# Performance work log

Hardware: AMD Instinct MI355X
Metric: run time of the kernel (lower is better)

The kernel has to match this reference:

```python
import jax, jax.numpy as jnp
import numpy as np

NUM_HEADS = 4
HEAD_DIM = 64
BN_EPS = 1e-5

def _leaky_relu(x, slope=0.2):
    return jnp.where(x >= 0, x, slope * x)

def _gat_conv(x, W, a_src, a_dst, src, dst):
    # x: [N, F_in], W: [F_out, F_in], a_*: [H, D]; edges src/dst: [E]
    N = x.shape[0]
    h = (x @ W.T).reshape(N, NUM_HEADS, HEAD_DIM)          # [N, H, D]
    s_src = jnp.einsum('nhd,hd->nh', h, a_src)              # [N, H]
    s_dst = jnp.einsum('nhd,hd->nh', h, a_dst)              # [N, H]
    e = _leaky_relu(s_src[src] + s_dst[dst])                # [E, H]
    # segment softmax over edges grouped by dst; torch index_reduce_ starts
    # from zeros (include_self=True) -> max with 0
    e_max = jnp.maximum(jax.ops.segment_max(e, dst, num_segments=N), 0.0)
    e_exp = jnp.exp(e - e_max[dst])                         # [E, H]
    e_sum = jax.ops.segment_sum(e_exp, dst, num_segments=N) # [N, H]
    alpha = e_exp / jnp.maximum(e_sum[dst], 1e-9)           # [E, H]
    msg = h[src] * alpha[..., None]                         # [E, H, D]
    out = jax.ops.segment_sum(msg, dst, num_segments=N)     # [N, H, D]
    return out.reshape(N, NUM_HEADS * HEAD_DIM)

def _bn_eval(x, gamma, beta, mean, var):
    return (x - mean) * jax.lax.rsqrt(var + BN_EPS) * gamma + beta

def _elu(x):
    return jnp.where(x > 0, x, jnp.expm1(x))

def setup_inputs() -> dict:
    key = jax.random.key(0)
    ks = jax.random.split(key, 12)
    N, E, IN, HID, OUT = 50000, 500000, 256, 256, 64
    s = 0.05
    return {
        'x': jax.random.normal(ks[0], (N, IN), jnp.float32),
        'edge_index': jax.random.randint(ks[1], (2, E), 0, N, jnp.int64),
        'W1': jax.random.normal(ks[2], (HID, IN), jnp.float32) * s,
        'a_src1': jax.random.normal(ks[3], (NUM_HEADS, HEAD_DIM), jnp.float32) * s,
        'a_dst1': jax.random.normal(ks[4], (NUM_HEADS, HEAD_DIM), jnp.float32) * s,
        'bn1_gamma': jnp.ones((HID,), jnp.float32),
        'bn1_beta': jnp.zeros((HID,), jnp.float32),
        'bn1_mean': jnp.zeros((HID,), jnp.float32),
        'bn1_var': jnp.ones((HID,), jnp.float32),
        'W2': jax.random.normal(ks[5], (HID, HID), jnp.float32) * s,
        'a_src2': jax.random.normal(ks[6], (NUM_HEADS, HEAD_DIM), jnp.float32) * s,
        'a_dst2': jax.random.normal(ks[7], (NUM_HEADS, HEAD_DIM), jnp.float32) * s,
        'bn2_gamma': jnp.ones((HID,), jnp.float32),
        'bn2_beta': jnp.zeros((HID,), jnp.float32),
        'bn2_mean': jnp.zeros((HID,), jnp.float32),
        'bn2_var': jnp.ones((HID,), jnp.float32),
        'Wc': jax.random.normal(ks[8], (OUT, HID), jnp.float32) * s,
        'bc': jnp.zeros((OUT,), jnp.float32),
    }

def reference(x, edge_index, W1, a_src1, a_dst1, bn1_gamma, bn1_beta, bn1_mean, bn1_var,
              W2, a_src2, a_dst2, bn2_gamma, bn2_beta, bn2_mean, bn2_var, Wc, bc):
    src, dst = edge_index[0], edge_index[1]
    h = _gat_conv(x, W1, a_src1, a_dst1, src, dst)
    h = _elu(_bn_eval(h, bn1_gamma, bn1_beta, bn1_mean, bn1_var))
    h = _gat_conv(h, W2, a_src2, a_dst2, src, dst)
    h = _elu(_bn_eval(h, bn2_gamma, bn2_beta, bn2_mean, bn2_var))
    return h @ Wc.T + bc
```

## Files before the change

kernel.cpp:

```cpp
#include <hip/hip_runtime.h>

typedef __attribute__((ext_vector_type(8))) short short8;
typedef __attribute__((ext_vector_type(4))) float f32x4;

#define FF 256
#define NHEAD 4
#define HDIM 64
#define LDS_PITCH 264

__device__ __forceinline__ float bf2f(unsigned short u) {
  union { unsigned u; float f; } v; v.u = ((unsigned)u) << 16; return v.f;
}
__device__ __forceinline__ unsigned short f2bf(float f) {
  union { unsigned u; float f; } v; v.f = f;
  unsigned r = v.u + 0x7FFFu + ((v.u >> 16) & 1u);
  return (unsigned short)(r >> 16);
}

__device__ __forceinline__ short8 loadA8(const unsigned short* p) {
  return *(const short8*)p;
}
__device__ __forceinline__ short8 loadA8(const float* p) {
  f32x4 a = *(const f32x4*)p;
  f32x4 b = *(const f32x4*)(p + 4);
  short8 r;
  r[0] = (short)f2bf(a.x); r[1] = (short)f2bf(a.y);
  r[2] = (short)f2bf(a.z); r[3] = (short)f2bf(a.w);
  r[4] = (short)f2bf(b.x); r[5] = (short)f2bf(b.y);
  r[6] = (short)f2bf(b.z); r[7] = (short)f2bf(b.w);
  return r;
}

__global__ __launch_bounds__(256) void cvtw_kernel(
    const float* __restrict__ p0, int n0, const float* __restrict__ p1, int n1,
    const float* __restrict__ p2, int n2,
    unsigned short* __restrict__ o0, unsigned short* __restrict__ o1,
    unsigned short* __restrict__ o2, int* __restrict__ deg, int nz4) {
  int i = blockIdx.x * 256 + threadIdx.x;
  const float* in;
  unsigned short* out;
  int idx;
  if (i < n0) { in = p0; out = o0; idx = i; }
  else if (i < n0 + n1) { in = p1; out = o1; idx = i - n0; }
  else if (i < n0 + n1 + n2) { in = p2; out = o2; idx = i - n0 - n1; }
  else {
    int z = i - n0 - n1 - n2;
    if (z < nz4) ((int4*)deg)[z] = int4{0, 0, 0, 0};
    return;
  }
  f32x4 v = ((const f32x4*)in)[idx];
  ushort4 o;
  o.x = f2bf(v.x); o.y = f2bf(v.y); o.z = f2bf(v.z); o.w = f2bf(v.w);
  ((ushort4*)out)[idx] = o;
}

__global__ void hist_kernel(const int* __restrict__ dst, int* __restrict__ deg,
                            int E, int N) {
  int i = blockIdx.x * blockDim.x + threadIdx.x;
  if (i < E) {
    int d = dst[i];
    if ((unsigned)d < (unsigned)N) atomicAdd(&deg[d], 1);
  }
}

__global__ __launch_bounds__(256) void scan_chunks(const int* __restrict__ deg,
                                                   int* __restrict__ excl,
                                                   int* __restrict__ csum, int N) {
  __shared__ int s[256];
  int t = threadIdx.x;
  int base = blockIdx.x * 1024 + t * 4;
  int v[4];
  int sum = 0;
#pragma unroll
  for (int i = 0; i < 4; ++i) {
    v[i] = (base + i < N) ? deg[base + i] : 0;
    sum += v[i];
  }
  s[t] = sum;
  __syncthreads();
  for (int off = 1; off < 256; off <<= 1) {
    int x = (t >= off) ? s[t - off] : 0;
    __syncthreads();
    s[t] += x;
    __syncthreads();
  }
  int run = s[t] - sum;
#pragma unroll
  for (int i = 0; i < 4; ++i) {
    if (base + i < N) excl[base + i] = run;
    run += v[i];
  }
  if (t == 255) csum[blockIdx.x] = s[255];
}

__global__ void finalize_rows(const int* __restrict__ excl, const int* __restrict__ csum,
                              int* __restrict__ row_start, int* __restrict__ cursor,
                              int N, int E) {
  int i = blockIdx.x * blockDim.x + threadIdx.x;
  if (i < N) {
    int chunk = i >> 10;
    int pre = 0;
    for (int k = 0; k < chunk; ++k) pre += csum[k];
    int v = excl[i] + pre;
    row_start[i] = v;
    cursor[i] = v;
  }
  if (i == 0) row_start[N] = E;
}

__global__ void scatter_kernel(const int* __restrict__ src, const int* __restrict__ dst,
                               int* __restrict__ cursor, int* __restrict__ sorted_src,
                               int E, int N) {
  int i = blockIdx.x * blockDim.x + threadIdx.x;
  if (i < E) {
    int d = dst[i];
    int s = src[i];
    if ((unsigned)d < (unsigned)N) {
      int p = atomicAdd(&cursor[d], 1);
      if ((unsigned)p < (unsigned)E)
        sorted_src[p] = ((unsigned)s < (unsigned)N) ? s : 0;
    }
  }
}

template <typename AT>
__global__ __launch_bounds__(256) void gemm_main(const AT* __restrict__ A,
                                                 const unsigned short* __restrict__ B,
                                                 unsigned short* __restrict__ Cb,
                                                 const float* __restrict__ a_src,
                                                 const float* __restrict__ a_dst,
                                                 float* __restrict__ sS,
                                                 float* __restrict__ sD,
                                                 int M) {
  __shared__ unsigned short Atile[64 * LDS_PITCH];
  const int K = 256;
  int tid = threadIdx.x;
  int wave = tid >> 6;
  int lane = tid & 63;
  int row0w = blockIdx.x * 64;
  int col0 = wave * 64;
  int lr = lane & 15;
  int quad = lane >> 4;

  short8 breg[4][8];
  {
    const unsigned short* Bp0 = B + (size_t)(col0 + lr) * K + quad * 8;
#pragma unroll
    for (int t = 0; t < 4; ++t)
#pragma unroll
      for (int kk = 0; kk < 8; ++kk)
        breg[t][kk] = *(const short8*)(Bp0 + (size_t)(16 * t) * K + kk * 32);
  }

  {
#pragma unroll
    for (int pass = 0; pass < 8; ++pass) {
      int c = tid + pass * 256;
      int row = c >> 5;
      int col8 = (c & 31) * 8;
      int grow = row0w + row;
      if (grow >= M) grow = M - 1;
      short8 v = loadA8(A + (size_t)grow * K + col8);
      *(short8*)(&Atile[row * LDS_PITCH + col8]) = v;
    }
  }
  __syncthreads();

  f32x4 acc[4][4];
#pragma unroll
  for (int rt = 0; rt < 4; ++rt)
#pragma unroll
    for (int t = 0; t < 4; ++t) acc[rt][t] = f32x4{0, 0, 0, 0};

#pragma unroll
  for (int kk = 0; kk < 8; ++kk) {
    short8 a[4];
#pragma unroll
    for (int rt = 0; rt < 4; ++rt)
      a[rt] = *(const short8*)(&Atile[(rt * 16 + lr) * LDS_PITCH + quad * 8 + kk * 32]);
#pragma unroll
    for (int rt = 0; rt < 4; ++rt)
#pragma unroll
      for (int t = 0; t < 4; ++t)
        acc[rt][t] = __builtin_amdgcn_mfma_f32_16x16x32_bf16(a[rt], breg[t][kk], acc[rt][t], 0, 0, 0);
  }

#pragma unroll
  for (int rt = 0; rt < 4; ++rt) {
#pragma unroll
    for (int t = 0; t < 4; ++t) {
#pragma unroll
      for (int r = 0; r < 4; ++r) {
        int row = row0w + rt * 16 + quad * 4 + r;
        if (row < M) {
          int col = col0 + 16 * t + lr;
          Cb[(size_t)row * FF + col] = f2bf(acc[rt][t][r]);
        }
      }
    }
  }

  {
    float asv[4], adv[4];
#pragma unroll
    for (int t = 0; t < 4; ++t) {
      asv[t] = a_src[col0 + 16 * t + lr];
      adv[t] = a_dst[col0 + 16 * t + lr];
    }
#pragma unroll
    for (int rt = 0; rt < 4; ++rt) {
#pragma unroll
      for (int r = 0; r < 4; ++r) {
        float ps = acc[rt][0][r] * asv[0] + acc[rt][1][r] * asv[1] +
                   acc[rt][2][r] * asv[2] + acc[rt][3][r] * asv[3];
        float pd = acc[rt][0][r] * adv[0] + acc[rt][1][r] * adv[1] +
                   acc[rt][2][r] * adv[2] + acc[rt][3][r] * adv[3];
#pragma unroll
        for (int sft = 1; sft < 16; sft <<= 1) {
          ps += __shfl_xor(ps, sft);
          pd += __shfl_xor(pd, sft);
        }
        if (lr == 0) {
          int row = row0w + rt * 16 + quad * 4 + r;
          if (row < M) {
            sS[row * NHEAD + wave] = ps;
            sD[row * NHEAD + wave] = pd;
          }
        }
      }
    }
  }
}

__global__ __launch_bounds__(256) void gemm_head(const unsigned short* __restrict__ A,
                                                 const unsigned short* __restrict__ B,
                                                 float* __restrict__ Cf,
                                                 const float* __restrict__ bias,
                                                 int M) {
  const int K = 256;
  int wave = threadIdx.x >> 6;
  int lane = threadIdx.x & 63;
  int row0w = blockIdx.x * 256 + wave * 64;
  if (row0w >= M) return;
  int lr = lane & 15;
  int quad = lane >> 4;

  short8 breg[4][8];
  {
    const unsigned short* Bp0 = B + (size_t)lr * K + quad * 8;
#pragma unroll
    for (int t = 0; t < 4; ++t)
#pragma unroll
      for (int kk = 0; kk < 8; ++kk)
        breg[t][kk] = *(const short8*)(Bp0 + (size_t)(16 * t) * K + kk * 32);
  }

  const unsigned short* Aps[4];
#pragma unroll
  for (int rt = 0; rt < 4; ++rt) {
    int arow = row0w + rt * 16 + lr;
    if (arow >= M) arow = M - 1;
    Aps[rt] = A + (size_t)arow * K + quad * 8;
  }

  f32x4 acc[4][4];
#pragma unroll
  for (int rt = 0; rt < 4; ++rt)
#pragma unroll
    for (int t = 0; t < 4; ++t) acc[rt][t] = f32x4{0, 0, 0, 0};

#pragma unroll
  for (int kk = 0; kk < 8; ++kk) {
    short8 a[4];
#pragma unroll
    for (int rt = 0; rt < 4; ++rt) a[rt] = *(const short8*)(Aps[rt] + kk * 32);
#pragma unroll
    for (int rt = 0; rt < 4; ++rt)
#pragma unroll
      for (int t = 0; t < 4; ++t)
        acc[rt][t] = __builtin_amdgcn_mfma_f32_16x16x32_bf16(a[rt], breg[t][kk], acc[rt][t], 0, 0, 0);
  }

#pragma unroll
  for (int rt = 0; rt < 4; ++rt) {
#pragma unroll
    for (int t = 0; t < 4; ++t) {
#pragma unroll
      for (int r = 0; r < 4; ++r) {
        int row = row0w + rt * 16 + quad * 4 + r;
        if (row < M) {
          int col = 16 * t + lr;
          Cf[(size_t)row * 64 + col] = acc[rt][t][r] + bias[col];
        }
      }
    }
  }
}

__global__ __launch_bounds__(256) void aggregate_kernel(
    const unsigned short* __restrict__ hprev, const float* __restrict__ sS,
    const float* __restrict__ sD, const int* __restrict__ row_start,
    const int* __restrict__ sorted_src, const float* __restrict__ gamma,
    const float* __restrict__ beta, const float* __restrict__ mean,
    const float* __restrict__ var, unsigned short* __restrict__ hout, int N) {
  int wave = threadIdx.x >> 6;
  int lane = threadIdx.x & 63;
  int n = blockIdx.x * 4 + wave;
  if (n >= N) return;
  int hh = lane >> 4;
  int slot = lane & 15;
  int f0 = lane * 4;
  int srcBase = lane & 48;
  int jb = row_start[n];
  int je = row_start[n + 1];
  int jlast = je - 1;
  float sdv = sD[n * NHEAD + hh];
  float l = 0.f;
  float o0 = 0.f, o1 = 0.f, o2 = 0.f, o3 = 0.f;

  for (int c = jb; c < je; c += 16) {
    int j = c + slot;
    int jc = (j < jlast) ? j : jlast;
    int s = sorted_src[jc];
    float e = sS[s * NHEAD + hh] + sdv;
    e = (e >= 0.f) ? e : 0.2f * e;
    float w = (j < je) ? __expf(e) : 0.f;
    l += w;

    {
      uint2 u[8];
#pragma unroll
      for (int k = 0; k < 8; ++k) {
        int sk = __shfl(s, srcBase + k, 64);
        u[k] = *(const uint2*)(hprev + (size_t)sk * FF + f0);
      }
#pragma unroll
      for (int k = 0; k < 8; ++k) {
        float a = __shfl(w, srcBase + k, 64);
        o0 += a * __uint_as_float(u[k].x << 16);
        o1 += a * __uint_as_float(u[k].x & 0xffff0000u);
        o2 += a * __uint_as_float(u[k].y << 16);
        o3 += a * __uint_as_float(u[k].y & 0xffff0000u);
      }
    }
    if (c + 8 < je) {
      uint2 u[8];
#pragma unroll
      for (int k = 8; k < 16; ++k) {
        int sk = __shfl(s, srcBase + k, 64);
        u[k - 8] = *(const uint2*)(hprev + (size_t)sk * FF + f0);
      }
#pragma unroll
      for (int k = 8; k < 16; ++k) {
        float a = __shfl(w, srcBase + k, 64);
        o0 += a * __uint_as_float(u[k - 8].x << 16);
        o1 += a * __uint_as_float(u[k - 8].x & 0xffff0000u);
        o2 += a * __uint_as_float(u[k - 8].y << 16);
        o3 += a * __uint_as_float(u[k - 8].y & 0xffff0000u);
      }
    }
  }

  l += __shfl_xor(l, 1);
  l += __shfl_xor(l, 2);
  l += __shfl_xor(l, 4);
  l += __shfl_xor(l, 8);
  float li = 1.f / fmaxf(l, 1e-9f);

  f32x4 g = *(const f32x4*)(gamma + f0);
  f32x4 b = *(const f32x4*)(beta + f0);
  f32x4 mu = *(const f32x4*)(mean + f0);
  f32x4 vr = *(const f32x4*)(var + f0);
  float v0 = (o0 * li - mu.x) * rsqrtf(vr.x + 1e-5f) * g.x + b.x;
  float v1 = (o1 * li - mu.y) * rsqrtf(vr.y + 1e-5f) * g.y + b.y;
  float v2 = (o2 * li - mu.z) * rsqrtf(vr.z + 1e-5f) * g.z + b.z;
  float v3 = (o3 * li - mu.w) * rsqrtf(vr.w + 1e-5f) * g.w + b.w;
  v0 = (v0 > 0.f) ? v0 : expm1f(v0);
  v1 = (v1 > 0.f) ? v1 : expm1f(v1);
  v2 = (v2 > 0.f) ? v2 : expm1f(v2);
  v3 = (v3 > 0.f) ? v3 : expm1f(v3);
  ushort4 ov;
  ov.x = f2bf(v0); ov.y = f2bf(v1); ov.z = f2bf(v2); ov.w = f2bf(v3);
  *(ushort4*)(hout + (size_t)n * FF + f0) = ov;
}

extern "C" void kernel_launch(void* const* d_in, const int* in_sizes, int n_in,
                              void* d_out, int out_size, void* d_ws, size_t ws_size,
                              hipStream_t stream) {
  const float* x   = (const float*)d_in[0];
  const int* ei    = (const int*)d_in[1];
  const float* W1  = (const float*)d_in[2];
  const float* as1 = (const float*)d_in[3];
  const float* ad1 = (const float*)d_in[4];
  const float* g1  = (const float*)d_in[5];
  const float* b1  = (const float*)d_in[6];
  const float* m1  = (const float*)d_in[7];
  const float* v1  = (const float*)d_in[8];
  const float* W2  = (const float*)d_in[9];
  const float* as2 = (const float*)d_in[10];
  const float* ad2 = (const float*)d_in[11];
  const float* g2  = (const float*)d_in[12];
  const float* b2  = (const float*)d_in[13];
  const float* m2  = (const float*)d_in[14];
  const float* v2  = (const float*)d_in[15];
  const float* Wc  = (const float*)d_in[16];
  const float* bc  = (const float*)d_in[17];

  const int N = in_sizes[0] / FF;
  const int E = in_sizes[1] / 2;
  const int* srcIdx = ei;
  const int* dstIdx = ei + E;

  char* ws = (char*)d_ws;
  size_t off = 0;
  auto take = [&](size_t bytes) -> void* {
    void* p = ws + off;
    off += (bytes + 255) & ~(size_t)255;
    return p;
  };
  int* deg        = (int*)take((size_t)((N + 3) & ~3) * 4);
  int* excl       = (int*)take((size_t)N * 4);
  int* csum       = (int*)take(256 * 4);
  int* row_start  = (int*)take(((size_t)N + 1) * 4);
  int* cursor     = (int*)take((size_t)N * 4);
  int* sorted_src = (int*)take((size_t)E * 4);
  float* sS       = (float*)take((size_t)N * NHEAD * 4);
  float* sD       = (float*)take((size_t)N * NHEAD * 4);
  unsigned short* hpre = (unsigned short*)take((size_t)N * FF * 2);
  unsigned short* hact = (unsigned short*)take((size_t)N * FF * 2);
  unsigned short* w1b  = (unsigned short*)take((size_t)FF * FF * 2);
  unsigned short* w2b  = (unsigned short*)take((size_t)FF * FF * 2);
  unsigned short* wcb  = (unsigned short*)take((size_t)64 * FF * 2);

  const int tpb = 256;

  {
    int n0 = (FF * FF) / 4, n1 = (FF * FF) / 4, n2 = (64 * FF) / 4;
    int nz4 = (N + 3) / 4;
    int tot = n0 + n1 + n2 + nz4;
    cvtw_kernel<<<(tot + tpb - 1) / tpb, tpb, 0, stream>>>(W1, n0, W2, n1, Wc, n2,
                                                           w1b, w2b, wcb, deg, nz4);
  }

  hist_kernel<<<(E + tpb - 1) / tpb, tpb, 0, stream>>>(dstIdx, deg, E, N);
  int nchunks = (N + 1023) / 1024;
  scan_chunks<<<nchunks, 256, 0, stream>>>(deg, excl, csum, N);
  finalize_rows<<<(N + tpb - 1) / tpb, tpb, 0, stream>>>(excl, csum, row_start, cursor, N, E);
  scatter_kernel<<<(E + tpb - 1) / tpb, tpb, 0, stream>>>(srcIdx, dstIdx, cursor, sorted_src, E, N);

  int aggBlocks = (N + 3) / 4;
  int gemmBlocks = (N + 63) / 64;
  int headBlocks = (N + 255) / 256;

  gemm_main<float><<<gemmBlocks, 256, 0, stream>>>(x, w1b, hpre, as1, ad1, sS, sD, N);
  aggregate_kernel<<<aggBlocks, 256, 0, stream>>>(hpre, sS, sD, row_start, sorted_src,
                                                  g1, b1, m1, v1, hact, N);
  gemm_main<unsigned short><<<gemmBlocks, 256, 0, stream>>>(hact, w2b, hpre, as2, ad2,
                                                            sS, sD, N);
  aggregate_kernel<<<aggBlocks, 256, 0, stream>>>(hpre, sS, sD, row_start, sorted_src,
                                                  g2, b2, m2, v2, hact, N);
  gemm_head<<<headBlocks, 256, 0, stream>>>(hact, wcb, (float*)d_out, bc, N);
}
```

Before: 335.1 us.

## Split B register preload in halves, shrink head blocks, pack aggregate FMAs

```diff
diff --git a/kernel.cpp b/kernel.cpp
--- a/kernel.cpp
+++ b/kernel.cpp
@@ -2,6 +2,7 @@
 
 typedef __attribute__((ext_vector_type(8))) short short8;
 typedef __attribute__((ext_vector_type(4))) float f32x4;
+typedef __attribute__((ext_vector_type(2))) float f32x2;
 
 #define FF 256
 #define NHEAD 4
@@ -142,16 +143,6 @@
   int lr = lane & 15;
   int quad = lane >> 4;
 
-  short8 breg[4][8];
-  {
-    const unsigned short* Bp0 = B + (size_t)(col0 + lr) * K + quad * 8;
-#pragma unroll
-    for (int t = 0; t < 4; ++t)
-#pragma unroll
-      for (int kk = 0; kk < 8; ++kk)
-        breg[t][kk] = *(const short8*)(Bp0 + (size_t)(16 * t) * K + kk * 32);
-  }
-
   {
 #pragma unroll
     for (int pass = 0; pass < 8; ++pass) {
@@ -166,6 +157,8 @@
   }
   __syncthreads();
 
+  const unsigned short* Bp0 = B + (size_t)(col0 + lr) * K + quad * 8;
+
   f32x4 acc[4][4];
 #pragma unroll
   for (int rt = 0; rt < 4; ++rt)
@@ -173,16 +166,27 @@
     for (int t = 0; t < 4; ++t) acc[rt][t] = f32x4{0, 0, 0, 0};
 
 #pragma unroll
-  for (int kk = 0; kk < 8; ++kk) {
-    short8 a[4];
-#pragma unroll
-    for (int rt = 0; rt < 4; ++rt)
-      a[rt] = *(const short8*)(&Atile[(rt * 16 + lr) * LDS_PITCH + quad * 8 + kk * 32]);
-#pragma unroll
-    for (int rt = 0; rt < 4; ++rt)
-#pragma unroll
-      for (int t = 0; t < 4; ++t)
-        acc[rt][t] = __builtin_amdgcn_mfma_f32_16x16x32_bf16(a[rt], breg[t][kk], acc[rt][t], 0, 0, 0);
+  for (int half = 0; half < 2; ++half) {
+    short8 breg[4][4];
+#pragma unroll
+    for (int t = 0; t < 4; ++t)
+#pragma unroll
+      for (int kk = 0; kk < 4; ++kk)
+        breg[t][kk] = *(const short8*)(Bp0 + (size_t)(16 * t) * K + (half * 4 + kk) * 32);
+#pragma unroll
+    for (int kk = 0; kk < 4; ++kk) {
+      short8 a[4];
+#pragma unroll
+      for (int rt = 0; rt < 4; ++rt)
+        a[rt] = *(const short8*)(&Atile[(rt * 16 + lr) * LDS_PITCH + quad * 8 +
+                                        (half * 4 + kk) * 32]);
+#pragma unroll
+      for (int rt = 0; rt < 4; ++rt)
+#pragma unroll
+        for (int t = 0; t < 4; ++t)
+          acc[rt][t] = __builtin_amdgcn_mfma_f32_16x16x32_bf16(a[rt], breg[t][kk],
+                                                               acc[rt][t], 0, 0, 0);
+    }
   }
 
 #pragma unroll
@@ -232,15 +236,14 @@
   }
 }
 
-__global__ __launch_bounds__(256) void gemm_head(const unsigned short* __restrict__ A,
-                                                 const unsigned short* __restrict__ B,
-                                                 float* __restrict__ Cf,
-                                                 const float* __restrict__ bias,
-                                                 int M) {
+__global__ __launch_bounds__(64) void gemm_head(const unsigned short* __restrict__ A,
+                                                const unsigned short* __restrict__ B,
+                                                float* __restrict__ Cf,
+                                                const float* __restrict__ bias,
+                                                int M) {
   const int K = 256;
-  int wave = threadIdx.x >> 6;
   int lane = threadIdx.x & 63;
-  int row0w = blockIdx.x * 256 + wave * 64;
+  int row0w = blockIdx.x * 64;
   if (row0w >= M) return;
   int lr = lane & 15;
   int quad = lane >> 4;
@@ -316,7 +319,7 @@
   int jlast = je - 1;
   float sdv = sD[n * NHEAD + hh];
   float l = 0.f;
-  float o0 = 0.f, o1 = 0.f, o2 = 0.f, o3 = 0.f;
+  f32x2 oA = {0.f, 0.f}, oB = {0.f, 0.f};
 
   for (int c = jb; c < je; c += 16) {
     int j = c + slot;
@@ -337,10 +340,11 @@
 #pragma unroll
       for (int k = 0; k < 8; ++k) {
         float a = __shfl(w, srcBase + k, 64);
-        o0 += a * __uint_as_float(u[k].x << 16);
-        o1 += a * __uint_as_float(u[k].x & 0xffff0000u);
-        o2 += a * __uint_as_float(u[k].y << 16);
-        o3 += a * __uint_as_float(u[k].y & 0xffff0000u);
+        f32x2 av = {a, a};
+        f32x2 dx = {__uint_as_float(u[k].x << 16), __uint_as_float(u[k].x & 0xffff0000u)};
+        f32x2 dy = {__uint_as_float(u[k].y << 16), __uint_as_float(u[k].y & 0xffff0000u)};
+        oA += av * dx;
+        oB += av * dy;
       }
     }
     if (c + 8 < je) {
@@ -353,10 +357,13 @@
 #pragma unroll
       for (int k = 8; k < 16; ++k) {
         float a = __shfl(w, srcBase + k, 64);
-        o0 += a * __uint_as_float(u[k - 8].x << 16);
-        o1 += a * __uint_as_float(u[k - 8].x & 0xffff0000u);
-        o2 += a * __uint_as_float(u[k - 8].y << 16);
-        o3 += a * __uint_as_float(u[k - 8].y & 0xffff0000u);
+        f32x2 av = {a, a};
+        f32x2 dx = {__uint_as_float(u[k - 8].x << 16),
+                    __uint_as_float(u[k - 8].x & 0xffff0000u)};
+        f32x2 dy = {__uint_as_float(u[k - 8].y << 16),
+                    __uint_as_float(u[k - 8].y & 0xffff0000u)};
+        oA += av * dx;
+        oB += av * dy;
       }
     }
   }
@@ -367,6 +374,7 @@
   l += __shfl_xor(l, 8);
   float li = 1.f / fmaxf(l, 1e-9f);
 
+  float o0 = oA.x, o1 = oA.y, o2 = oB.x, o3 = oB.y;
   f32x4 g = *(const f32x4*)(gamma + f0);
   f32x4 b = *(const f32x4*)(beta + f0);
   f32x4 mu = *(const f32x4*)(mean + f0);
@@ -450,7 +458,6 @@
 
   int aggBlocks = (N + 3) / 4;
   int gemmBlocks = (N + 63) / 64;
-  int headBlocks = (N + 255) / 256;
 
   gemm_main<float><<<gemmBlocks, 256, 0, stream>>>(x, w1b, hpre, as1, ad1, sS, sD, N);
   aggregate_kernel<<<aggBlocks, 256, 0, stream>>>(hpre, sS, sD, row_start, sorted_src,
@@ -459,5 +466,5 @@
                                                             sS, sD, N);
   aggregate_kernel<<<aggBlocks, 256, 0, stream>>>(hpre, sS, sD, row_start, sorted_src,
                                                   g2, b2, m2, v2, hact, N);
-  gemm_head<<<headBlocks, 256, 0, stream>>>(hact, wcb, (float*)d_out, bc, N);
-}
+  gemm_head<<<gemmBlocks, 64, 0, stream>>>(hact, wcb, (float*)d_out, bc, N);
+}
```

After: 352.2 us. 1.05x slower.
